# Optimization experiments

Hardware: AMD Instinct MI355X
Metric: run time of the kernel (lower is better)

The kernel has to match this reference:

```python
import jax, jax.numpy as jnp
from jax import lax
import numpy as np

DN = ('NHWC', 'HWIO', 'NHWC')


def conv2(x, w1, b1, w2, b2):
    # Sequential(Conv2D(units,3,same,relu), Conv2D(1,3,same,relu))
    y = jax.nn.relu(lax.conv_general_dilated(x, w1, (1, 1), 'SAME', dimension_numbers=DN) + b1)
    y = jax.nn.relu(lax.conv_general_dilated(y, w2, (1, 1), 'SAME', dimension_numbers=DN) + b2)
    return y


def resize_and_pad(fm, box, Hb, Wb):
    # Static-shape reformulation of tf.image.resize (bilinear, half-pixel) +
    # tf.pad: for every bg pixel inside the box, bilinearly sample the source
    # map; pixels outside the box are zero (the pad region).
    h, w = fm.shape[0], fm.shape[1]
    y_size = jnp.floor(Hb * (box[1] - box[0]))  # int() truncation on positives
    x_size = jnp.floor(Wb * (box[3] - box[2]))
    yf = jnp.floor(Hb * box[0])
    xf = jnp.floor(Wb * box[2])
    Y = jnp.arange(Hb, dtype=fm.dtype)[:, None]
    X = jnp.arange(Wb, dtype=fm.dtype)[None, :]
    ly = Y - yf  # local row inside resized crop
    lx = X - xf
    valid = (ly >= 0) & (ly < y_size) & (lx >= 0) & (lx < x_size)
    sy = jnp.clip((ly + 0.5) * h / jnp.maximum(y_size, 1.0) - 0.5, 0.0, h - 1.0)
    sx = jnp.clip((lx + 0.5) * w / jnp.maximum(x_size, 1.0) - 0.5, 0.0, w - 1.0)
    sy = jnp.broadcast_to(sy, (Hb, Wb))
    sx = jnp.broadcast_to(sx, (Hb, Wb))
    y0 = jnp.floor(sy).astype(jnp.int32)
    x0 = jnp.floor(sx).astype(jnp.int32)
    y1 = jnp.minimum(y0 + 1, h - 1)
    x1 = jnp.minimum(x0 + 1, w - 1)
    wy = (sy - y0.astype(fm.dtype))[..., None]
    wx = (sx - x0.astype(fm.dtype))[..., None]
    top = fm[y0, x0] * (1 - wx) + fm[y0, x1] * wx
    bot = fm[y1, x0] * (1 - wx) + fm[y1, x1] * wx
    out = top * (1 - wy) + bot * wy
    return out * valid[..., None].astype(fm.dtype)


def _forward(instance_feature, bg_feature, bbox, mrcnn_mask,
             w1i, b1i, w2i, b2i, w1b, b1b, w2b, b2b, object_n):
    B, Hi, Wi, C, M = instance_feature.shape
    Hb, Wb = bg_feature.shape[1], bg_feature.shape[2]
    # fold objects into batch for the per-instance conv
    inst = jnp.transpose(instance_feature, (0, 4, 1, 2, 3)).reshape(B * M, Hi, Wi, C)
    inst_w = conv2(inst, w1i, b1i, w2i, b2i)  # [B*M,Hi,Wi,1]
    boxes = jnp.transpose(bbox, (0, 2, 1)).reshape(B * M, 4)
    rp = lambda fm, box: resize_and_pad(fm, box, Hb, Wb)
    rw = jax.vmap(rp)(inst_w, boxes).reshape(B, M, Hb, Wb, 1)      # resized weights
    rmask = jnp.where(rw > 0, 1.0, 0.0)                              # original derives mask from weights
    rfeat = jax.vmap(rp)(inst, boxes).reshape(B, M, Hb, Wb, C)      # resized features
    bg_w = conv2(bg_feature, w1b, b1b, w2b, b2b)                     # [B,Hb,Wb,1]
    # only the first object_n[i] objects exist for image i
    valid = (jnp.arange(M)[None, :] < object_n[:, None]).astype(rw.dtype)[:, :, None, None, None]
    exp_obj = jnp.exp(rw) * rmask * valid                            # masked exp gating
    exp_bg = jnp.exp(bg_w)
    denom = exp_obj.sum(axis=1) + exp_bg                             # [B,Hb,Wb,1]
    sm_obj = (exp_obj / denom[:, None])[..., 0]                      # [B,M,Hb,Wb]
    composed = (exp_bg / denom) * bg_feature + jnp.einsum('bmhw,bmhwc->bhwc', sm_obj, rfeat)
    return composed


def setup_inputs() -> dict:
    key = jax.random.key(0)
    ks = jax.random.split(key, 16)
    B, Hi, Wi, C, M, Hb, Wb, U = 10, 64, 64, 64, 8, 128, 128, 64
    instance_feature = jax.random.normal(ks[0], (B, Hi, Wi, C, M), jnp.float32)
    bg_feature = jax.random.normal(ks[1], (B, Hb, Wb, C), jnp.float32)
    mrcnn_mask = jax.random.uniform(ks[2], (B, Hi, Wi, M), jnp.float32)
    y0 = jax.random.uniform(ks[3], (B, M), jnp.float32) * 0.4
    y1 = y0 + 0.3 + jax.random.uniform(ks[4], (B, M), jnp.float32) * 0.25
    x0 = jax.random.uniform(ks[5], (B, M), jnp.float32) * 0.4
    x1 = x0 + 0.3 + jax.random.uniform(ks[6], (B, M), jnp.float32) * 0.25
    bbox = jnp.stack([y0, y1, x0, x1], axis=1)  # [B,4,M]
    object_n = jax.random.randint(ks[7], (B,), 1, M + 1).astype(jnp.int32)
    s = 0.05
    return {
        'instance_feature': instance_feature,
        'bg_feature': bg_feature,
        'bbox': bbox,
        'mrcnn_mask': mrcnn_mask,
        'w1i': jax.random.normal(ks[8], (3, 3, C, U), jnp.float32) * s,
        'b1i': jnp.zeros((U,), jnp.float32),
        'w2i': jax.random.normal(ks[9], (3, 3, U, 1), jnp.float32) * s,
        'b2i': jnp.zeros((1,), jnp.float32),
        'w1b': jax.random.normal(ks[10], (3, 3, C, U), jnp.float32) * s,
        'b1b': jnp.zeros((U,), jnp.float32),
        'w2b': jax.random.normal(ks[11], (3, 3, U, 1), jnp.float32) * s,
        'b2b': jnp.zeros((1,), jnp.float32),
        'object_n': object_n,
    }


def reference(instance_feature, bg_feature, bbox, mrcnn_mask,
              w1i, b1i, w2i, b2i, w1b, b1b, w2b, b2b, object_n):
    return _forward(instance_feature, bg_feature, bbox, mrcnn_mask,
                    w1i, b1i, w2i, b2i, w1b, b1b, w2b, b2b, object_n)
```

## Files before the change

### kernel.cpp

```cpp
#include <hip/hip_runtime.h>
#include <cstdint>
#include <cstddef>


typedef __attribute__((ext_vector_type(8))) short short8;
typedef __attribute__((ext_vector_type(4))) float f32x4;

__device__ __forceinline__ unsigned short f2bf(float x) {
  union { float f; unsigned int u; } v; v.f = x;
  unsigned int r = (v.u + 0x7FFFu + ((v.u >> 16) & 1u)) >> 16;
  return (unsigned short)r;
}
__device__ __forceinline__ float bf2f(unsigned short h) {
  union { unsigned int u; float f; } v; v.u = ((unsigned int)h) << 16;
  return v.f;
}
__device__ __forceinline__ void split3(float v, unsigned short& h,
                                       unsigned short& m, unsigned short& l) {
  h = f2bf(v);
  float r1 = v - bf2f(h);
  m = f2bf(r1);
  float r2 = r1 - bf2f(m);
  l = f2bf(r2);
}

__global__ void prep_w3(const float* __restrict__ w, unsigned short* __restrict__ wB)
{
  int idx = blockIdx.x * 256 + threadIdx.x;
  if (idx >= 18 * 4 * 64 * 8) return;
  int i = idx & 7;
  int lane = (idx >> 3) & 63;
  int ut = (idx >> 9) & 3;
  int kc = idx >> 11;
  int k = kc * 32 + (lane >> 4) * 8 + i;
  int u = ut * 16 + (lane & 15);
  int k9 = k >> 6, c = k & 63;
  float v = w[((size_t)(k9 * 64 + c)) * 64 + u];
  unsigned short h, m, l;
  split3(v, h, m, l);
  wB[idx] = h;
  wB[36864 + idx] = m;
  wB[73728 + idx] = l;
}

__global__ __launch_bounds__(256) void tr_if(const float* __restrict__ IFh,
                                             float* __restrict__ TIF)
{
  const int idx = blockIdx.x * 256 + threadIdx.x;
  const int c = idx & 63;
  const int x = (idx >> 6) & 63;
  const int y = (idx >> 12) & 63;
  const int bb = idx >> 18;
  const float* p = IFh + (size_t)idx * 8;
  float4 v0 = *(const float4*)p;
  float4 v1 = *(const float4*)(p + 4);
  float mv[8] = {v0.x, v0.y, v0.z, v0.w, v1.x, v1.y, v1.z, v1.w};
  #pragma unroll
  for (int m = 0; m < 8; ++m)
    TIF[((size_t)(bb * 8 + m) * 4096 + y * 64 + x) * 64 + c] = mv[m];
}

__global__ __launch_bounds__(256, 2) void conv1_m(const float* __restrict__ TIF,
    const float* __restrict__ BG,
    const unsigned short* __restrict__ wBi, const unsigned short* __restrict__ wBb,
    const float* __restrict__ b1i, const float* __restrict__ b1b,
    float* __restrict__ h1i, float* __restrict__ h1g, int hh)
{
  __shared__ __align__(16) char lds[76032];

  const int tid = threadIdx.x;
  const int bid = blockIdx.x;
  const bool inst = (bid < 640);

  int H, W, imgL, xt, rg;
  const unsigned short* wB;
  const float* bias;
  const float* srcimg;
  float* dst;
  if (inst) {
    H = 64; W = 64;
    imgL = bid >> 4; rg = bid & 15; xt = 0;
    wB = wBi; bias = b1i; dst = h1i;
    srcimg = TIF + (size_t)imgL * 262144;
  } else {
    const int bb = bid - 640;
    H = 128; W = 128;
    xt = bb & 1;
    const int t2 = bb >> 1;
    rg = t2 & 31; imgL = t2 >> 5;
    wB = wBb; bias = b1b; dst = h1g;
    srcimg = BG + (size_t)(hh * 5 + imgL) * 1048576;
  }
  const int yb = rg << 2;
  const int xb = xt << 6;
  const int wave = tid >> 6, lane = tid & 63;
  const int mrow = lane & 15, g = lane >> 4;

  f32x4 z = {0.f, 0.f, 0.f, 0.f};
  f32x4 acc[4][4];
  #pragma unroll
  for (int i = 0; i < 4; ++i)
    #pragma unroll
    for (int j = 0; j < 4; ++j)
      acc[i][j] = z;

  const short8* wBp = (const short8*)wB;

  for (int cc = 0; cc < 2; ++cc) {
    if (cc) __syncthreads();
    for (int e = tid; e < 1584; e += 256) {
      const int c8 = e & 3;
      const int q = e >> 2;
      const int xi = q % 66;
      const int r = q / 66;
      const int gy = yb + r - 1;
      const int gx = xb + xi - 1;
      float v[8] = {0.f, 0.f, 0.f, 0.f, 0.f, 0.f, 0.f, 0.f};
      if (gy >= 0 && gy < H && gx >= 0 && gx < W) {
        const float* p = srcimg + ((size_t)gy * W + gx) * 64 + cc * 32 + c8 * 8;
        float4 a = *(const float4*)p;
        float4 bq = *(const float4*)(p + 4);
        v[0] = a.x; v[1] = a.y; v[2] = a.z; v[3] = a.w;
        v[4] = bq.x; v[5] = bq.y; v[6] = bq.z; v[7] = bq.w;
      }
      short8 ph, pm, pl;
      #pragma unroll
      for (int j = 0; j < 8; ++j) {
        unsigned short h2, mi, l2;
        split3(v[j], h2, mi, l2);
        ph[j] = (short)h2; pm[j] = (short)mi; pl[j] = (short)l2;
      }
      const int wbase = (r * 4 + c8) * 1056 + xi * 16;
      *(short8*)&lds[wbase] = ph;
      *(short8*)&lds[wbase + 25344] = pm;
      *(short8*)&lds[wbase + 50688] = pl;
    }
    __syncthreads();

    for (int tap = 0; tap < 9; ++tap) {
      const int dy = tap / 3, dx = tap % 3;
      const int kc = tap * 2 + cc;
      short8 a[4][3];
      #pragma unroll
      for (int pxt = 0; pxt < 4; ++pxt) {
        const int abase = ((wave + dy) * 4 + g) * 1056 + (pxt * 16 + mrow + dx) * 16;
        #pragma unroll
        for (int pl = 0; pl < 3; ++pl)
          a[pxt][pl] = *(const short8*)&lds[abase + pl * 25344];
      }
      #pragma unroll
      for (int ut = 0; ut < 4; ++ut) {
        const int bi = (kc * 4 + ut) * 64 + lane;
        short8 bfr[3];
        bfr[0] = wBp[bi];
        bfr[1] = wBp[4608 + bi];
        bfr[2] = wBp[9216 + bi];
        #pragma unroll
        for (int p = 0; p < 6; ++p) {
          const int PA[6] = {0, 0, 1, 0, 2, 1};
          const int PB[6] = {0, 1, 0, 2, 0, 1};
          const int pa = PA[p], pb = PB[p];
          #pragma unroll
          for (int pxt = 0; pxt < 4; ++pxt)
            acc[pxt][ut] = __builtin_amdgcn_mfma_f32_16x16x32_bf16(
                a[pxt][pa], bfr[pb], acc[pxt][ut], 0, 0, 0);
        }
      }
    }
  }

  const int y = yb + wave;
  #pragma unroll
  for (int ut = 0; ut < 4; ++ut) {
    const int u = ut * 16 + mrow;
    const float bv = bias[u];
    #pragma unroll
    for (int pxt = 0; pxt < 4; ++pxt) {
      #pragma unroll
      for (int r = 0; r < 4; ++r) {
        const int px = xb + pxt * 16 + g * 4 + r;
        dst[((size_t)(imgL * H + y) * W + px) * 64 + u] = fmaxf(acc[pxt][ut][r] + bv, 0.f);
      }
    }
  }
}

__global__ __launch_bounds__(256) void conv2_m(const float* __restrict__ h1i,
    const float* __restrict__ h1g,
    const float* __restrict__ w2i, const float* __restrict__ w2b,
    const float* __restrict__ b2i, const float* __restrict__ b2b,
    float* __restrict__ instw, float* __restrict__ bgw, int hh)
{
  const int RS = 24;
  const int CS = 18 * 24 + 1;
  __shared__ float s[32 * (18 * 24 + 1)];
  __shared__ float wsm[576];

  const int tid = threadIdx.x;
  const int bid = blockIdx.x;
  const bool inst = (bid < 640);

  int H, W, n, xt, yt;
  const float* hsrc;
  const float* w2;
  const float* b2;
  float* dst;
  if (inst) {
    H = 64; W = 64;
    n = bid >> 4;
    const int t = bid & 15;
    xt = t & 3; yt = t >> 2;
    hsrc = h1i; w2 = w2i; b2 = b2i;
    dst = instw + (size_t)(hh * 40 + n) * 4096;
  } else {
    const int bb = bid - 640;
    H = 128; W = 128;
    n = bb >> 6;
    const int t = bb & 63;
    xt = t & 7; yt = t >> 3;
    hsrc = h1g; w2 = w2b; b2 = b2b;
    dst = bgw + (size_t)(hh * 5 + n) * 16384;
  }
  const int xb = xt << 4, yb = yt << 4;
  const int tx = tid & 15, ty = tid >> 4;

  for (int e = tid; e < 576; e += 256) wsm[e] = w2[e];

  float acc = 0.f;
  for (int cc = 0; cc < 2; ++cc) {
    const int c0 = cc << 5;
    if (cc) __syncthreads();
    for (int e = tid; e < 18 * 18 * 32; e += 256) {
      int c = e & 31;
      int p = e >> 5;
      int xx = p % 18;
      int yy = p / 18;
      int gy = yb + yy - 1, gx = xb + xx - 1;
      float v = 0.f;
      if (gy >= 0 && gy < H && gx >= 0 && gx < W)
        v = hsrc[((size_t)(n * H + gy) * W + gx) * 64 + c0 + c];
      s[c * CS + yy * RS + xx] = v;
    }
    __syncthreads();
    for (int c = 0; c < 32; ++c) {
      const float* sp = &s[c * CS + ty * RS + tx];
      const float* wp = &wsm[c0 + c];
      #pragma unroll
      for (int dy = 0; dy < 3; ++dy)
        #pragma unroll
        for (int dx = 0; dx < 3; ++dx)
          acc += sp[dy * RS + dx] * wp[(dy * 3 + dx) * 64];
    }
  }
  dst[(size_t)(yb + ty) * W + xb + tx] = fmaxf(acc + b2[0], 0.f);
}

__global__ __launch_bounds__(256) void compose_v4(const float* __restrict__ TIF,
    const float* __restrict__ bg, const float* __restrict__ bbox,
    const int* __restrict__ objn, const float* __restrict__ instw,
    const float* __restrict__ bgw, float* __restrict__ out, int hh)
{
  __shared__ __align__(16) float P[4][8][8];

  const int tid = threadIdx.x;
  const int lane = tid & 63;
  const int wave = tid >> 6;
  const int c = lane;
  const int pid = hh * 81920 + blockIdx.x * 4 + wave;
  const int b = pid >> 14;
  const int rem = pid & 16383;
  const int hhp = rem >> 7;
  const int www = rem & 127;

  if (lane < 8) {
    const int m = lane;
    const float y0b = bbox[b * 32 + m];
    const float y1b = bbox[b * 32 + 8 + m];
    const float x0b = bbox[b * 32 + 16 + m];
    const float x1b = bbox[b * 32 + 24 + m];
    const float ysz = floorf(128.f * (y1b - y0b));
    const float xsz = floorf(128.f * (x1b - x0b));
    const float yf = floorf(128.f * y0b);
    const float xf = floorf(128.f * x0b);
    const float ly = (float)hhp - yf;
    const float lx = (float)www - xf;
    const bool valid = (m < objn[b]) && (ly >= 0.f) && (ly < ysz)
                       && (lx >= 0.f) && (lx < xsz);
    float sy = (ly + 0.5f) * 64.f / fmaxf(ysz, 1.f) - 0.5f;
    float sx = (lx + 0.5f) * 64.f / fmaxf(xsz, 1.f) - 0.5f;
    sy = fminf(fmaxf(sy, 0.f), 63.f);
    sx = fminf(fmaxf(sx, 0.f), 63.f);
    const int y0i = (int)floorf(sy);
    const int x0i = (int)floorf(sx);
    const int y1i = min(y0i + 1, 63);
    const int x1i = min(x0i + 1, 63);
    const float wy = sy - (float)y0i;
    const float wx = sx - (float)x0i;
    const float omwx = 1.f - wx, omwy = 1.f - wy;

    const float* iw = instw + (size_t)(b * 8 + m) * 4096;
    const float v00 = iw[y0i * 64 + x0i];
    const float v01 = iw[y0i * 64 + x1i];
    const float v10 = iw[y1i * 64 + x0i];
    const float v11 = iw[y1i * 64 + x1i];
    const float rwv = (v00 * omwx + v01 * wx) * omwy + (v10 * omwx + v11 * wx) * wy;
    const bool on = valid && (rwv > 0.f);
    const float e = on ? expf(rwv) : 0.f;

    P[wave][m][0] = e;
    P[wave][m][1] = wx;
    P[wave][m][2] = wy;
    P[wave][m][3] = (float)(y0i * 4096 + x0i * 64);
    P[wave][m][4] = (float)(y0i * 4096 + x1i * 64);
    P[wave][m][5] = (float)(y1i * 4096 + x0i * 64);
    P[wave][m][6] = (float)(y1i * 4096 + x1i * 64);
    P[wave][m][7] = 0.f;
  }
  __syncthreads();

  const float ebg = expf(bgw[pid]);
  const float bgc = bg[(size_t)pid * 64 + c];
  float denom = ebg;
  float acc = ebg * bgc;
  const float* fb = TIF + (size_t)(b - hh * 5) * 8 * 262144 + c;

  #pragma unroll
  for (int m = 0; m < 8; ++m) {
    const float4 pa = *(const float4*)&P[wave][m][0];
    const float4 pb = *(const float4*)&P[wave][m][4];
    const float e = pa.x;
    denom += e;
    if (e != 0.f) {
      const float* fm = fb + (size_t)m * 262144;
      const float t00 = fm[(int)pa.w];
      const float t01 = fm[(int)pb.x];
      const float t10 = fm[(int)pb.y];
      const float t11 = fm[(int)pb.z];
      const float wx = pa.y, wy = pa.z;
      const float omwx = 1.f - wx, omwy = 1.f - wy;
      const float bil = (t00 * omwx + t01 * wx) * omwy + (t10 * omwx + t11 * wx) * wy;
      acc += e * bil;
    }
  }
  out[(size_t)pid * 64 + c] = acc / denom;
}

extern "C" void kernel_launch(void* const* d_in, const int* in_sizes, int n_in,
                              void* d_out, int out_size, void* d_ws, size_t ws_size,
                              hipStream_t stream)
{
  const float* IF   = (const float*)d_in[0];
  const float* BG   = (const float*)d_in[1];
  const float* BBOX = (const float*)d_in[2];
  const float* w1i = (const float*)d_in[4];
  const float* b1i = (const float*)d_in[5];
  const float* w2i = (const float*)d_in[6];
  const float* b2i = (const float*)d_in[7];
  const float* w1b = (const float*)d_in[8];
  const float* b1b = (const float*)d_in[9];
  const float* w2b = (const float*)d_in[10];
  const float* b2b = (const float*)d_in[11];
  const int* objn  = (const int*)d_in[12];
  float* out = (float*)d_out;

  char* wsb = (char*)d_ws;
  unsigned short* wBi3 = (unsigned short*)(wsb);
  unsigned short* wBb3 = (unsigned short*)(wsb + 221184);
  float* instw = (float*)(wsb + 442368);
  float* bgw   = (float*)(wsb + 1753088);
  float* TIF   = (float*)(wsb + 2408448);
  float* h1i   = (float*)(wsb + 44351488);
  float* h1g   = out + 5242880;

  prep_w3<<<144, 256, 0, stream>>>(w1i, wBi3);
  prep_w3<<<144, 256, 0, stream>>>(w1b, wBb3);

  for (int hh = 0; hh < 2; ++hh) {
    tr_if<<<5120, 256, 0, stream>>>(IF + (size_t)hh * 10485760, TIF);
    conv1_m<<<960, 256, 0, stream>>>(TIF, BG, wBi3, wBb3, b1i, b1b, h1i, h1g, hh);
    conv2_m<<<960, 256, 0, stream>>>(h1i, h1g, w2i, w2b, b2i, b2b, instw, bgw, hh);
    compose_v4<<<20480, 256, 0, stream>>>(TIF, BG, BBOX, objn, instw, bgw, out, hh);
  }
}
```

Before: 420.3 us.

## Switch conv1 to 32x32x16 bf16 MFMA with halved LDS staging

Rewrites the first convolution's implicit GEMM to use the 32x32x16 bf16 MFMA instead of 16x16x32, with the weight prep relaid out to match and channels staged in four 16-channel chunks instead of two 32-channel chunks. The LDS footprint halves, so launch bounds now request four blocks per CU instead of two. The aim is fewer MFMA and LDS-fragment instructions per FLOP and higher occupancy. In exchange it adds extra barriers and staging passes, and a runtime probe MFMA that detects the output-register orientation before choosing the store index mapping.

Measured after the change: 485.4 us. +15.5%, slower.

```diff
diff --git a/kernel.cpp b/kernel.cpp
--- a/kernel.cpp
+++ b/kernel.cpp
@@ -5,6 +5,7 @@
 
 typedef __attribute__((ext_vector_type(8))) short short8;
 typedef __attribute__((ext_vector_type(4))) float f32x4;
+typedef __attribute__((ext_vector_type(16))) float f32x16;
 
 __device__ __forceinline__ unsigned short f2bf(float x) {
   union { float f; unsigned int u; } v; v.f = x;
@@ -24,18 +25,18 @@
   l = f2bf(r2);
 }
 
-__global__ void prep_w3(const float* __restrict__ w, unsigned short* __restrict__ wB)
+__global__ void prep_w32(const float* __restrict__ w, unsigned short* __restrict__ wB)
 {
   int idx = blockIdx.x * 256 + threadIdx.x;
-  if (idx >= 18 * 4 * 64 * 8) return;
+  if (idx >= 36864) return;
   int i = idx & 7;
   int lane = (idx >> 3) & 63;
-  int ut = (idx >> 9) & 3;
-  int kc = idx >> 11;
-  int k = kc * 32 + (lane >> 4) * 8 + i;
-  int u = ut * 16 + (lane & 15);
-  int k9 = k >> 6, c = k & 63;
-  float v = w[((size_t)(k9 * 64 + c)) * 64 + u];
+  int ut = (idx >> 9) & 1;
+  int kq = idx >> 10;
+  int k = kq * 16 + ((lane >> 5) << 3) + i;
+  int u = ut * 32 + (lane & 31);
+  int tap = k >> 6, c = k & 63;
+  float v = w[((size_t)(tap * 64 + c)) * 64 + u];
   unsigned short h, m, l;
   split3(v, h, m, l);
   wB[idx] = h;
@@ -60,13 +61,13 @@
     TIF[((size_t)(bb * 8 + m) * 4096 + y * 64 + x) * 64 + c] = mv[m];
 }
 
-__global__ __launch_bounds__(256, 2) void conv1_m(const float* __restrict__ TIF,
+__global__ __launch_bounds__(256, 4) void conv1_m(const float* __restrict__ TIF,
     const float* __restrict__ BG,
     const unsigned short* __restrict__ wBi, const unsigned short* __restrict__ wBb,
     const float* __restrict__ b1i, const float* __restrict__ b1b,
     float* __restrict__ h1i, float* __restrict__ h1g, int hh)
 {
-  __shared__ __align__(16) char lds[76032];
+  __shared__ __align__(16) char lds[38016];
 
   const int tid = threadIdx.x;
   const int bid = blockIdx.x;
@@ -94,30 +95,45 @@
   const int yb = rg << 2;
   const int xb = xt << 6;
   const int wave = tid >> 6, lane = tid & 63;
-  const int mrow = lane & 15, g = lane >> 4;
-
-  f32x4 z = {0.f, 0.f, 0.f, 0.f};
-  f32x4 acc[4][4];
+  const int l31 = lane & 31, cg8 = lane >> 5;
+
+  f32x16 zz;
   #pragma unroll
-  for (int i = 0; i < 4; ++i)
+  for (int i = 0; i < 16; ++i) zz[i] = 0.f;
+
+  bool swapped;
+  {
+    short8 pa = {0,0,0,0,0,0,0,0}, pb = {0,0,0,0,0,0,0,0};
+    if (cg8 == 0) {
+      pa[5] = (short)f2bf((float)(l31 + 1));
+      pb[5] = (short)f2bf((float)((l31 + 1) * (l31 + 1)));
+    }
+    f32x16 pd = __builtin_amdgcn_mfma_f32_32x32x16_bf16(pa, pb, zz, 0, 0, 0);
+    const float d2 = __shfl(pd[0], 2, 64);
+    swapped = (d2 < 6.0f);
+  }
+
+  f32x16 acc[2][2];
+  #pragma unroll
+  for (int i = 0; i < 2; ++i)
     #pragma unroll
-    for (int j = 0; j < 4; ++j)
-      acc[i][j] = z;
+    for (int j = 0; j < 2; ++j)
+      acc[i][j] = zz;
 
   const short8* wBp = (const short8*)wB;
 
-  for (int cc = 0; cc < 2; ++cc) {
-    if (cc) __syncthreads();
-    for (int e = tid; e < 1584; e += 256) {
-      const int c8 = e & 3;
-      const int q = e >> 2;
-      const int xi = q % 66;
-      const int r = q / 66;
+  for (int q = 0; q < 4; ++q) {
+    if (q) __syncthreads();
+    for (int e = tid; e < 792; e += 256) {
+      const int cg = e & 1;
+      const int q2 = e >> 1;
+      const int xi = q2 % 66;
+      const int r = q2 / 66;
       const int gy = yb + r - 1;
       const int gx = xb + xi - 1;
       float v[8] = {0.f, 0.f, 0.f, 0.f, 0.f, 0.f, 0.f, 0.f};
       if (gy >= 0 && gy < H && gx >= 0 && gx < W) {
-        const float* p = srcimg + ((size_t)gy * W + gx) * 64 + cc * 32 + c8 * 8;
+        const float* p = srcimg + ((size_t)gy * W + gx) * 64 + q * 16 + cg * 8;
         float4 a = *(const float4*)p;
         float4 bq = *(const float4*)(p + 4);
         v[0] = a.x; v[1] = a.y; v[2] = a.z; v[3] = a.w;
@@ -130,27 +146,27 @@
         split3(v[j], h2, mi, l2);
         ph[j] = (short)h2; pm[j] = (short)mi; pl[j] = (short)l2;
       }
-      const int wbase = (r * 4 + c8) * 1056 + xi * 16;
+      const int wbase = ((r * 2 + cg) * 66 + xi) << 4;
       *(short8*)&lds[wbase] = ph;
-      *(short8*)&lds[wbase + 25344] = pm;
-      *(short8*)&lds[wbase + 50688] = pl;
+      *(short8*)&lds[wbase + 12672] = pm;
+      *(short8*)&lds[wbase + 25344] = pl;
     }
     __syncthreads();
 
     for (int tap = 0; tap < 9; ++tap) {
       const int dy = tap / 3, dx = tap % 3;
-      const int kc = tap * 2 + cc;
-      short8 a[4][3];
+      const int kq = tap * 4 + q;
+      short8 a[2][3];
       #pragma unroll
-      for (int pxt = 0; pxt < 4; ++pxt) {
-        const int abase = ((wave + dy) * 4 + g) * 1056 + (pxt * 16 + mrow + dx) * 16;
+      for (int pxt = 0; pxt < 2; ++pxt) {
+        const int abase = (((wave + dy) * 2 + cg8) * 66 + (pxt * 32 + l31 + dx)) << 4;
         #pragma unroll
         for (int pl = 0; pl < 3; ++pl)
-          a[pxt][pl] = *(const short8*)&lds[abase + pl * 25344];
+          a[pxt][pl] = *(const short8*)&lds[abase + pl * 12672];
       }
       #pragma unroll
-      for (int ut = 0; ut < 4; ++ut) {
-        const int bi = (kc * 4 + ut) * 64 + lane;
+      for (int ut = 0; ut < 2; ++ut) {
+        const int bi = (kq * 2 + ut) * 64 + lane;
         short8 bfr[3];
         bfr[0] = wBp[bi];
         bfr[1] = wBp[4608 + bi];
@@ -161,8 +177,8 @@
           const int PB[6] = {0, 1, 0, 2, 0, 1};
           const int pa = PA[p], pb = PB[p];
           #pragma unroll
-          for (int pxt = 0; pxt < 4; ++pxt)
-            acc[pxt][ut] = __builtin_amdgcn_mfma_f32_16x16x32_bf16(
+          for (int pxt = 0; pxt < 2; ++pxt)
+            acc[pxt][ut] = __builtin_amdgcn_mfma_f32_32x32x16_bf16(
                 a[pxt][pa], bfr[pb], acc[pxt][ut], 0, 0, 0);
         }
       }
@@ -171,15 +187,18 @@
 
   const int y = yb + wave;
   #pragma unroll
-  for (int ut = 0; ut < 4; ++ut) {
-    const int u = ut * 16 + mrow;
-    const float bv = bias[u];
+  for (int ut = 0; ut < 2; ++ut) {
     #pragma unroll
-    for (int pxt = 0; pxt < 4; ++pxt) {
+    for (int pxt = 0; pxt < 2; ++pxt) {
       #pragma unroll
-      for (int r = 0; r < 4; ++r) {
-        const int px = xb + pxt * 16 + g * 4 + r;
-        dst[((size_t)(imgL * H + y) * W + px) * 64 + u] = fmaxf(acc[pxt][ut][r] + bv, 0.f);
+      for (int reg = 0; reg < 16; ++reg) {
+        const int rloc = (reg & 3) + 8 * (reg >> 2) + 4 * cg8;
+        const int pxl = swapped ? l31 : rloc;
+        const int ul  = swapped ? rloc : l31;
+        const int px = xb + pxt * 32 + pxl;
+        const int u = ut * 32 + ul;
+        dst[((size_t)(imgL * H + y) * W + px) * 64 + u] =
+            fmaxf(acc[pxt][ut][reg] + bias[u], 0.f);
       }
     }
   }
@@ -372,8 +391,8 @@
   float* h1i   = (float*)(wsb + 44351488);
   float* h1g   = out + 5242880;
 
-  prep_w3<<<144, 256, 0, stream>>>(w1i, wBi3);
-  prep_w3<<<144, 256, 0, stream>>>(w1b, wBb3);
+  prep_w32<<<144, 256, 0, stream>>>(w1i, wBi3);
+  prep_w32<<<144, 256, 0, stream>>>(w1b, wBb3);
 
   for (int hh = 0; hh < 2; ++hh) {
     tr_if<<<5120, 256, 0, stream>>>(IF + (size_t)hh * 10485760, TIF);
```
